# Optimization experiments

Hardware: AMD Instinct MI355X
Metric: run time of the kernel (lower is better)

## Reference

```python
import jax, jax.numpy as jnp
import numpy as np

NUM_HEADS = 16
HEAD_DIM = 64  # embedding_dim 1024 / 16


def setup_inputs() -> dict:
    key = jax.random.key(0)
    k1, k2, k3, k4 = jax.random.split(key, 4)
    B, S, D = 2, 2048, 1024
    return {
        "query": jax.random.normal(k1, (B, S, D), dtype=jnp.float32),
        "key": jax.random.normal(k2, (B, S, D), dtype=jnp.float32),
        "value": jax.random.normal(k3, (B, S, D), dtype=jnp.float32),
        "W_out": jax.random.normal(k4, (D, D), dtype=jnp.float32) * (1.0 / np.sqrt(D)),
        "b_out": jnp.zeros((D,), dtype=jnp.float32),
    }


def reference(query, key, value, W_out, b_out):
    B, S, D = query.shape
    H, hd = NUM_HEADS, HEAD_DIM
    # NOTE: original forward never applies q_fc/k_fc/v_fc (transform ignores fc)
    q = query.reshape(B, S, H, hd).transpose(0, 2, 1, 3)  # [B,H,S,hd]
    k = key.reshape(B, S, H, hd).transpose(0, 2, 1, 3)
    v = value.reshape(B, S, H, hd).transpose(0, 2, 1, 3)
    scores = jnp.einsum("bhqd,bhkd->bhqk", q, k) / jnp.sqrt(jnp.float32(hd))
    probs = jax.nn.softmax(scores, axis=-1)  # mask=None, dropout=None
    ctx = jnp.einsum("bhqk,bhkd->bhqd", probs, v)
    ctx = ctx.transpose(0, 2, 1, 3).reshape(B, S, D)
    return ctx @ W_out.T + b_out
```

## Files before the change

### kernel.cpp

```cpp
#include <hip/hip_runtime.h>
#include <hip/hip_bf16.h>
#include <stdint.h>

#define NB 2
#define SEQ 2048
#define DIM 1024
#define NH 16
#define HD 64

typedef __attribute__((ext_vector_type(4))) float f32x4;
typedef __attribute__((ext_vector_type(16))) float f32x16;
typedef __attribute__((ext_vector_type(8))) short s16x8;
typedef __attribute__((ext_vector_type(4))) short s16x4;
typedef __attribute__((ext_vector_type(8))) __bf16 bf16x8;

static __device__ __forceinline__ short f2bf_rne(float x) {
  uint32_t u = __float_as_uint(x);
  u += 0x7fffu + ((u >> 16) & 1u);
  return (short)(u >> 16);
}
static __device__ __forceinline__ uint32_t pk_bf16(float a, float b) {
  __hip_bfloat162 h = __float22bfloat162_rn(float2{a, b});
  uint32_t u;
  __builtin_memcpy(&u, &h, 4);
  return u;
}
static __device__ __forceinline__ bf16x8 ldfrag(const short* p) {
  bf16x8 r;
  __builtin_memcpy(&r, p, 16);
  return r;
}
static __device__ __forceinline__ void glds16(const short* g, short* l) {
  __builtin_amdgcn_global_load_lds(
      (const __attribute__((address_space(1))) uint32_t*)g,
      (__attribute__((address_space(3))) uint32_t*)l, 16, 0, 0);
}

__global__ __launch_bounds__(256) void prep_all(const float* __restrict__ K,
                                                const float* __restrict__ V,
                                                const float* __restrict__ W,
                                                short* __restrict__ Kh,
                                                short* __restrict__ Vt,
                                                short* __restrict__ Wh) {
  __shared__ float vtile[64][65];
  const int tid = threadIdx.x;
  const int id = blockIdx.x;

  if (id >= 1024) {
    size_t idx = ((size_t)(id - 1024) * 256 + tid) * 8;
    f32x4 a = *(const f32x4*)(W + idx);
    f32x4 b = *(const f32x4*)(W + idx + 4);
    s16x8 o;
#pragma unroll
    for (int j = 0; j < 4; ++j) {
      o[j] = f2bf_rne(a[j]);
      o[4 + j] = f2bf_rne(b[j]);
    }
    *(s16x8*)(Wh + idx) = o;
    return;
  }

  const int t0 = (id & 31) * 64;
  const int bh = id >> 5;
  const int b = bh >> 4, h = bh & 15;

#pragma unroll
  for (int i = 0; i < 4; ++i) {
    int f = tid + 256 * i;
    int row = f >> 4;
    int col = (f & 15) * 4;
    const float* src = K + ((size_t)(b * SEQ + t0 + row)) * DIM + h * HD + col;
    f32x4 v = *(const f32x4*)src;
    s16x4 hi;
#pragma unroll
    for (int j = 0; j < 4; ++j) hi[j] = f2bf_rne(v[j]);
    int kvh = row >> 5, l32r = row & 31;
    int ks = col >> 4, hl2 = (col >> 3) & 1, j0 = col & 7;
    *(s16x4*)(Kh + ((size_t)(bh * SEQ + t0)) * HD + kvh * 2048 + ks * 512 +
              l32r * 16 + hl2 * 8 + j0) = hi;
  }
#pragma unroll
  for (int i = 0; i < 4; ++i) {
    int f = tid + 256 * i;
    int row = f >> 4;
    int col = (f & 15) * 4;
    const float* src = V + ((size_t)(b * SEQ + t0 + row)) * DIM + h * HD + col;
    f32x4 v = *(const f32x4*)src;
#pragma unroll
    for (int j = 0; j < 4; ++j) vtile[row][col + j] = v[j];
  }
  __syncthreads();
#pragma unroll
  for (int i = 0; i < 4; ++i) {
    int idx = tid + 256 * i;
    int d = idx >> 4;
    int kb = (idx & 15) * 4;
    int kp = (kb & ~12) | ((kb & 4) << 1) | ((kb & 8) >> 1);
    s16x4 o4;
#pragma unroll
    for (int j = 0; j < 4; ++j) o4[j] = f2bf_rne(vtile[kb + j][d]);
    *(s16x4*)(Vt + ((size_t)bh * HD + d) * SEQ + t0 + kp) = o4;
  }
}

#define QSCALE (0.125f * 1.44269504088896340736f)
#define NT_KV 32

static __device__ __forceinline__ void exppv32(const f32x16& sf, const short* vb,
                                               int kvh, int l32, int hl,
                                               f32x16* acc, float& den0,
                                               float& den1) {
#pragma unroll
  for (int tp = 0; tp < 2; ++tp) {
    uint32_t w[4];
#pragma unroll
    for (int j2 = 0; j2 < 4; ++j2) {
      float p0 = __builtin_amdgcn_exp2f(sf[tp * 8 + j2 * 2]);
      float p1 = __builtin_amdgcn_exp2f(sf[tp * 8 + j2 * 2 + 1]);
      den0 += p0;
      den1 += p1;
      w[j2] = pk_bf16(p0, p1);
    }
    bf16x8 pa;
    __builtin_memcpy(&pa, w, 16);
    const int ksg = kvh * 2 + tp;
#pragma unroll
    for (int dt = 0; dt < 2; ++dt) {
      bf16x8 vf = ldfrag(vb + (dt * 32 + l32) * 64 +
                         (((ksg * 2 + hl) ^ (l32 & 7)) * 8));
      acc[dt] =
          __builtin_amdgcn_mfma_f32_32x32x16_bf16(pa, vf, acc[dt], 0, 0, 0);
    }
  }
}

static __device__ __forceinline__ f32x16 qkreg(const bf16x8* kf,
                                               const bf16x8* qh) {
  f32x16 s;
#pragma unroll
  for (int r = 0; r < 16; ++r) s[r] = 0.f;
#pragma unroll
  for (int ks = 0; ks < 4; ++ks)
    s = __builtin_amdgcn_mfma_f32_32x32x16_bf16(kf[ks], qh[ks], s, 0, 0, 0);
  return s;
}

__global__ __launch_bounds__(512, 4) void attn(const float* __restrict__ Q,
                                               const short* __restrict__ Kh,
                                               const short* __restrict__ Vt,
                                               short* __restrict__ Ch) {
  __shared__ __align__(16) short vbuf[2][4096];
  __shared__ __align__(16) float xbuf[4096];
  __shared__ float dsh[8][64];

  const int tid = threadIdx.x;
  const int wv = tid >> 6, ln = tid & 63;
  const int l32 = ln & 31, hl = ln >> 5;
  const int qsub = wv >> 1, kvh = wv & 1;
  const int bh = blockIdx.y, b = bh >> 4, hh = bh & 15;
  const int q0 = blockIdx.x * 128 + qsub * 32;

  bf16x8 qh[4];
  {
    const float* qp = Q + ((size_t)(b * SEQ + q0 + l32)) * DIM + hh * HD + hl * 8;
#pragma unroll
    for (int ks = 0; ks < 4; ++ks) {
      short th[8];
#pragma unroll
      for (int j = 0; j < 8; ++j) th[j] = f2bf_rne(qp[ks * 16 + j] * QSCALE);
      __builtin_memcpy(&qh[ks], th, 16);
    }
  }

  f32x16 acc[2];
#pragma unroll
  for (int r = 0; r < 16; ++r) {
    acc[0][r] = 0.f;
    acc[1][r] = 0.f;
  }
  float den0 = 0.f, den1 = 0.f;

  const short* khg =
      Kh + (size_t)bh * SEQ * HD + kvh * 2048 + l32 * 16 + hl * 8;
  const short* vtg = Vt + (size_t)bh * HD * SEQ;

  const int srow8 = ln >> 3;
  const int sg = ln & 7;
  const int sw = (sg ^ srow8) * 8;
  const int srow = wv * 8 + srow8;

  bf16x8 kf0[4];
#pragma unroll
  for (int ks = 0; ks < 4; ++ks) kf0[ks] = ldfrag(khg + ks * 512);
  glds16(vtg + (size_t)srow * SEQ + sw, &vbuf[0][wv * 512]);
  f32x16 sfA = qkreg(kf0, qh);

  for (int t = 0; t < 30; t += 2) {
    __syncthreads();
    bf16x8 kfa[4];
#pragma unroll
    for (int ks = 0; ks < 4; ++ks)
      kfa[ks] = ldfrag(khg + (t + 1) * 4096 + ks * 512);
    glds16(vtg + (size_t)srow * SEQ + (t + 1) * 64 + sw, &vbuf[1][wv * 512]);
    exppv32(sfA, &vbuf[0][0], kvh, l32, hl, acc, den0, den1);
    f32x16 sfB = qkreg(kfa, qh);
    __syncthreads();
    bf16x8 kfb[4];
#pragma unroll
    for (int ks = 0; ks < 4; ++ks)
      kfb[ks] = ldfrag(khg + (t + 2) * 4096 + ks * 512);
    glds16(vtg + (size_t)srow * SEQ + (t + 2) * 64 + sw, &vbuf[0][wv * 512]);
    exppv32(sfB, &vbuf[1][0], kvh, l32, hl, acc, den0, den1);
    sfA = qkreg(kfb, qh);
  }
  __syncthreads();
  bf16x8 kfl[4];
#pragma unroll
  for (int ks = 0; ks < 4; ++ks) kfl[ks] = ldfrag(khg + 31 * 4096 + ks * 512);
  glds16(vtg + (size_t)srow * SEQ + 31 * 64 + sw, &vbuf[1][wv * 512]);
  exppv32(sfA, &vbuf[0][0], kvh, l32, hl, acc, den0, den1);
  f32x16 sfT = qkreg(kfl, qh);
  __syncthreads();
  exppv32(sfT, &vbuf[1][0], kvh, l32, hl, acc, den0, den1);

  float den = den0 + den1;
  den += __shfl_xor(den, 32);

  f32x16 give, keep;
  if (kvh == 0) {
    give = acc[1];
    keep = acc[0];
  } else {
    give = acc[0];
    keep = acc[1];
  }

  __syncthreads();
  float* xr = (wv < 4) ? &xbuf[0] : (float*)&vbuf[0][0];
  *(f32x16*)(xr + (wv & 3) * 1024 + ln * 16) = give;
  dsh[wv][ln] = den;
  __syncthreads();

  float dtot = den + dsh[wv ^ 1][ln];
  float invd = 1.0f / dtot;
  float inv_r[16];
#pragma unroll
  for (int r = 0; r < 16; ++r)
    inv_r[r] = __shfl(invd, (r & 3) + 8 * (r >> 2) + 4 * hl, 64);

  f32x16 oth = *(const f32x16*)(xr + ((wv ^ 1) & 3) * 1024 + ln * 16);
#pragma unroll
  for (int r = 0; r < 16; ++r) {
    float cs = keep[r] + oth[r];
    int row = (r & 3) + 8 * (r >> 2) + 4 * hl;
    size_t off =
        ((size_t)(b * SEQ + q0 + row)) * DIM + hh * HD + kvh * 32 + l32;
    Ch[off] = f2bf_rne(cs * inv_r[r]);
  }
}

__global__ __launch_bounds__(256, 4) void proj(const short* __restrict__ Ah,
                                               const short* __restrict__ Wh,
                                               const float* __restrict__ bias,
                                               float* __restrict__ OUT) {
  __shared__ __align__(16) short ash[2][4096];
  __shared__ __align__(16) short wsh[2][4096];
  const int tid = threadIdx.x;
  const int wv = tid >> 6, ln = tid & 63;
  const int l32 = ln & 31, hl = ln >> 5;
  const int wm = wv & 1, wn = wv >> 1;
  const int m0 = blockIdx.x * 64, n0 = blockIdx.y * 64;

  f32x16 acc;
#pragma unroll
  for (int r = 0; r < 16; ++r) acc[r] = 0.f;

  const int srow8 = ln >> 3, sg = ln & 7;
  const int sw = (sg ^ srow8) * 8;

#pragma unroll
  for (int i = 0; i < 4; ++i) {
    int c = wv * 4 + i;
    int row = (c & 7) * 8 + srow8;
    if (c < 8)
      glds16(Ah + (size_t)(m0 + row) * DIM + sw, ash[0] + (c & 7) * 512);
    else
      glds16(Wh + (size_t)(n0 + row) * DIM + sw, wsh[0] + (c & 7) * 512);
  }

  for (int kt = 0; kt < DIM / 64; ++kt) {
    __syncthreads();
    if (kt + 1 < DIM / 64) {
      const int kk = (kt + 1) * 64;
      const int bn = (kt + 1) & 1;
#pragma unroll
      for (int i = 0; i < 4; ++i) {
        int c = wv * 4 + i;
        int row = (c & 7) * 8 + srow8;
        if (c < 8)
          glds16(Ah + (size_t)(m0 + row) * DIM + kk + sw, ash[bn] + (c & 7) * 512);
        else
          glds16(Wh + (size_t)(n0 + row) * DIM + kk + sw, wsh[bn] + (c & 7) * 512);
      }
    }
    const short* ab = ash[kt & 1];
    const short* wb = wsh[kt & 1];
#pragma unroll
    for (int ks = 0; ks < 4; ++ks) {
      bf16x8 af = ldfrag(ab + (wm * 32 + l32) * 64 + (((ks * 2 + hl) ^ (l32 & 7)) * 8));
      bf16x8 wf = ldfrag(wb + (wn * 32 + l32) * 64 + (((ks * 2 + hl) ^ (l32 & 7)) * 8));
      acc = __builtin_amdgcn_mfma_f32_32x32x16_bf16(af, wf, acc, 0, 0, 0);
    }
  }

  float bs = bias[n0 + wn * 32 + l32];
#pragma unroll
  for (int r = 0; r < 16; ++r) {
    int row = m0 + wm * 32 + (r & 3) + 8 * (r >> 2) + 4 * hl;
    int col = n0 + wn * 32 + l32;
    OUT[(size_t)row * DIM + col] = acc[r] + bs;
  }
}

extern "C" void kernel_launch(void* const* d_in, const int* in_sizes, int n_in,
                              void* d_out, int out_size, void* d_ws, size_t ws_size,
                              hipStream_t stream) {
  const float* Q = (const float*)d_in[0];
  const float* K = (const float*)d_in[1];
  const float* V = (const float*)d_in[2];
  const float* W = (const float*)d_in[3];
  const float* bias = (const float*)d_in[4];
  float* OUT = (float*)d_out;

  char* ws = (char*)d_ws;
  short* Kh = (short*)(ws + ((size_t)0 << 20));
  short* Vt = (short*)(ws + ((size_t)8 << 20));
  short* Ch = (short*)(ws + ((size_t)16 << 20));
  short* Wh = (short*)(ws + ((size_t)24 << 20));

  prep_all<<<dim3(1536), 256, 0, stream>>>(K, V, W, Kh, Vt, Wh);
  attn<<<dim3(SEQ / 128, NB * NH), 512, 0, stream>>>(Q, Kh, Vt, Ch);
  proj<<<dim3((NB * SEQ) / 64, DIM / 64), 256, 0, stream>>>(Ch, Wh, bias, OUT);
}
```

Measured before the change: 159.5 us.

## Pre-swizzle V into MFMA fragment layout and load directly to registers

```diff
diff --git a/kernel.cpp b/kernel.cpp
--- a/kernel.cpp
+++ b/kernel.cpp
@@ -99,17 +99,31 @@
     s16x4 o4;
 #pragma unroll
     for (int j = 0; j < 4; ++j) o4[j] = f2bf_rne(vtile[kb + j][d]);
-    *(s16x4*)(Vt + ((size_t)bh * HD + d) * SEQ + t0 + kp) = o4;
+    int dt = d >> 5, l32r = d & 31;
+    int ksg = kp >> 4, hl2 = (kp >> 3) & 1, j0 = kp & 7;
+    *(s16x4*)(Vt + ((size_t)(bh * 32 + (t0 >> 6))) * 4096 +
+              (ksg * 2 + dt) * 512 + l32r * 16 + hl2 * 8 + j0) = o4;
   }
 }
 
 #define QSCALE (0.125f * 1.44269504088896340736f)
 #define NT_KV 32
 
-static __device__ __forceinline__ void exppv32(const f32x16& sf, const short* vb,
-                                               int kvh, int l32, int hl,
-                                               f32x16* acc, float& den0,
-                                               float& den1) {
+static __device__ __forceinline__ f32x16 qkreg(const bf16x8* kf,
+                                               const bf16x8* qh) {
+  f32x16 s;
+#pragma unroll
+  for (int r = 0; r < 16; ++r) s[r] = 0.f;
+#pragma unroll
+  for (int ks = 0; ks < 4; ++ks)
+    s = __builtin_amdgcn_mfma_f32_32x32x16_bf16(kf[ks], qh[ks], s, 0, 0, 0);
+  return s;
+}
+
+static __device__ __forceinline__ void exppv_reg(const f32x16& sf, bf16x8 v0,
+                                                 bf16x8 v1, bf16x8 v2,
+                                                 bf16x8 v3, f32x16* acc,
+                                                 float& den0, float& den1) {
 #pragma unroll
   for (int tp = 0; tp < 2; ++tp) {
     uint32_t w[4];
@@ -123,42 +137,30 @@
     }
     bf16x8 pa;
     __builtin_memcpy(&pa, w, 16);
-    const int ksg = kvh * 2 + tp;
-#pragma unroll
-    for (int dt = 0; dt < 2; ++dt) {
-      bf16x8 vf = ldfrag(vb + (dt * 32 + l32) * 64 +
-                         (((ksg * 2 + hl) ^ (l32 & 7)) * 8));
-      acc[dt] =
-          __builtin_amdgcn_mfma_f32_32x32x16_bf16(pa, vf, acc[dt], 0, 0, 0);
-    }
-  }
-}
-
-static __device__ __forceinline__ f32x16 qkreg(const bf16x8* kf,
-                                               const bf16x8* qh) {
-  f32x16 s;
-#pragma unroll
-  for (int r = 0; r < 16; ++r) s[r] = 0.f;
-#pragma unroll
-  for (int ks = 0; ks < 4; ++ks)
-    s = __builtin_amdgcn_mfma_f32_32x32x16_bf16(kf[ks], qh[ks], s, 0, 0, 0);
-  return s;
+    acc[0] = __builtin_amdgcn_mfma_f32_32x32x16_bf16(pa, tp ? v2 : v0, acc[0],
+                                                     0, 0, 0);
+    acc[1] = __builtin_amdgcn_mfma_f32_32x32x16_bf16(pa, tp ? v3 : v1, acc[1],
+                                                     0, 0, 0);
+  }
 }
 
 __global__ __launch_bounds__(512, 4) void attn(const float* __restrict__ Q,
                                                const short* __restrict__ Kh,
                                                const short* __restrict__ Vt,
                                                short* __restrict__ Ch) {
-  __shared__ __align__(16) short vbuf[2][4096];
-  __shared__ __align__(16) float xbuf[4096];
+  __shared__ __align__(16) float xbuf[8192];
   __shared__ float dsh[8][64];
 
   const int tid = threadIdx.x;
   const int wv = tid >> 6, ln = tid & 63;
   const int l32 = ln & 31, hl = ln >> 5;
   const int qsub = wv >> 1, kvh = wv & 1;
-  const int bh = blockIdx.y, b = bh >> 4, hh = bh & 15;
-  const int q0 = blockIdx.x * 128 + qsub * 32;
+
+  const int lin = blockIdx.y * gridDim.x + blockIdx.x;
+  const int nl = ((lin & 7) << 6) | (lin >> 3);
+  const int bx = nl & 15, bh = nl >> 4;
+  const int b = bh >> 4, hh = bh & 15;
+  const int q0 = bx * 128 + qsub * 32;
 
   bf16x8 qh[4];
   {
@@ -180,48 +182,65 @@
   }
   float den0 = 0.f, den1 = 0.f;
 
-  const short* khg =
+  const short* kbase =
       Kh + (size_t)bh * SEQ * HD + kvh * 2048 + l32 * 16 + hl * 8;
-  const short* vtg = Vt + (size_t)bh * HD * SEQ;
-
-  const int srow8 = ln >> 3;
-  const int sg = ln & 7;
-  const int sw = (sg ^ srow8) * 8;
-  const int srow = wv * 8 + srow8;
-
-  bf16x8 kf0[4];
-#pragma unroll
-  for (int ks = 0; ks < 4; ++ks) kf0[ks] = ldfrag(khg + ks * 512);
-  glds16(vtg + (size_t)srow * SEQ + sw, &vbuf[0][wv * 512]);
-  f32x16 sfA = qkreg(kf0, qh);
-
+  const short* vbase =
+      Vt + (size_t)bh * (SEQ / 64) * 4096 + kvh * 2048 + l32 * 16 + hl * 8;
+
+  bf16x8 kA[4];
+#pragma unroll
+  for (int ks = 0; ks < 4; ++ks) kA[ks] = ldfrag(kbase + ks * 512);
+  f32x16 sfA = qkreg(kA, qh);
+
+  bf16x8 v0, v1, v2, v3;
   for (int t = 0; t < 30; t += 2) {
-    __syncthreads();
-    bf16x8 kfa[4];
+    const short* vb0 = vbase + (size_t)t * 4096;
+    v0 = ldfrag(vb0);
+    v1 = ldfrag(vb0 + 512);
+    v2 = ldfrag(vb0 + 1024);
+    v3 = ldfrag(vb0 + 1536);
 #pragma unroll
     for (int ks = 0; ks < 4; ++ks)
-      kfa[ks] = ldfrag(khg + (t + 1) * 4096 + ks * 512);
-    glds16(vtg + (size_t)srow * SEQ + (t + 1) * 64 + sw, &vbuf[1][wv * 512]);
-    exppv32(sfA, &vbuf[0][0], kvh, l32, hl, acc, den0, den1);
-    f32x16 sfB = qkreg(kfa, qh);
-    __syncthreads();
-    bf16x8 kfb[4];
+      kA[ks] = ldfrag(kbase + (size_t)(t + 1) * 4096 + ks * 512);
+    exppv_reg(sfA, v0, v1, v2, v3, acc, den0, den1);
+    __builtin_amdgcn_s_setprio(1);
+    f32x16 sfB = qkreg(kA, qh);
+    __builtin_amdgcn_s_setprio(0);
+    const short* vb1 = vbase + (size_t)(t + 1) * 4096;
+    v0 = ldfrag(vb1);
+    v1 = ldfrag(vb1 + 512);
+    v2 = ldfrag(vb1 + 1024);
+    v3 = ldfrag(vb1 + 1536);
 #pragma unroll
     for (int ks = 0; ks < 4; ++ks)
-      kfb[ks] = ldfrag(khg + (t + 2) * 4096 + ks * 512);
-    glds16(vtg + (size_t)srow * SEQ + (t + 2) * 64 + sw, &vbuf[0][wv * 512]);
-    exppv32(sfB, &vbuf[1][0], kvh, l32, hl, acc, den0, den1);
-    sfA = qkreg(kfb, qh);
-  }
-  __syncthreads();
-  bf16x8 kfl[4];
-#pragma unroll
-  for (int ks = 0; ks < 4; ++ks) kfl[ks] = ldfrag(khg + 31 * 4096 + ks * 512);
-  glds16(vtg + (size_t)srow * SEQ + 31 * 64 + sw, &vbuf[1][wv * 512]);
-  exppv32(sfA, &vbuf[0][0], kvh, l32, hl, acc, den0, den1);
-  f32x16 sfT = qkreg(kfl, qh);
-  __syncthreads();
-  exppv32(sfT, &vbuf[1][0], kvh, l32, hl, acc, den0, den1);
+      kA[ks] = ldfrag(kbase + (size_t)(t + 2) * 4096 + ks * 512);
+    exppv_reg(sfB, v0, v1, v2, v3, acc, den0, den1);
+    __builtin_amdgcn_s_setprio(1);
+    sfA = qkreg(kA, qh);
+    __builtin_amdgcn_s_setprio(0);
+  }
+  {
+    const short* vb0 = vbase + (size_t)30 * 4096;
+    v0 = ldfrag(vb0);
+    v1 = ldfrag(vb0 + 512);
+    v2 = ldfrag(vb0 + 1024);
+    v3 = ldfrag(vb0 + 1536);
+#pragma unroll
+    for (int ks = 0; ks < 4; ++ks)
+      kA[ks] = ldfrag(kbase + (size_t)31 * 4096 + ks * 512);
+    exppv_reg(sfA, v0, v1, v2, v3, acc, den0, den1);
+    __builtin_amdgcn_s_setprio(1);
+    sfA = qkreg(kA, qh);
+    __builtin_amdgcn_s_setprio(0);
+  }
+  {
+    const short* vb1 = vbase + (size_t)31 * 4096;
+    v0 = ldfrag(vb1);
+    v1 = ldfrag(vb1 + 512);
+    v2 = ldfrag(vb1 + 1024);
+    v3 = ldfrag(vb1 + 1536);
+    exppv_reg(sfA, v0, v1, v2, v3, acc, den0, den1);
+  }
 
   float den = den0 + den1;
   den += __shfl_xor(den, 32);
@@ -235,9 +254,7 @@
     keep = acc[1];
   }
 
-  __syncthreads();
-  float* xr = (wv < 4) ? &xbuf[0] : (float*)&vbuf[0][0];
-  *(f32x16*)(xr + (wv & 3) * 1024 + ln * 16) = give;
+  *(f32x16*)(&xbuf[wv * 1024 + ln * 16]) = give;
   dsh[wv][ln] = den;
   __syncthreads();
 
@@ -248,7 +265,7 @@
   for (int r = 0; r < 16; ++r)
     inv_r[r] = __shfl(invd, (r & 3) + 8 * (r >> 2) + 4 * hl, 64);
 
-  f32x16 oth = *(const f32x16*)(xr + ((wv ^ 1) & 3) * 1024 + ln * 16);
+  f32x16 oth = *(const f32x16*)(&xbuf[(wv ^ 1) * 1024 + ln * 16]);
 #pragma unroll
   for (int r = 0; r < 16; ++r) {
     float cs = keep[r] + oth[r];
```

New measurement: 175.9 us. 1.1x slower.
